# Kernel tuning notes

Measured on AMD Instinct MI355X. Metric: run time of the kernel, lower is better.

Reference implementation:

```python
import jax, jax.numpy as jnp
import numpy as np

CORR_RANGE = 4
N_SEGMENT = 8
SIGMA = 0.1
BETA = 10.0


def setup_inputs() -> dict:
    key = jax.random.key(0)
    x = jax.random.normal(key, (64, 256, 56, 56), dtype=jnp.float32)
    return {"x": x}


def reference(x):
    d = CORR_RANGE
    K = 2 * d + 1  # 9
    bt, c, h, w = x.shape

    # x.detach() + F.normalize(p=2, dim=1)
    xd = jax.lax.stop_gradient(x)
    norm = jnp.sqrt(jnp.sum(xd * xd, axis=1, keepdims=True))
    x_m = xd / jnp.maximum(norm, 1e-12)

    # temporal shift: segment t gets features of segment t-1, segment 0 -> zeros
    x5 = x_m.reshape(-1, N_SEGMENT, c, h, w)
    x_post = jnp.concatenate([jnp.zeros_like(x5[:, :1]), x5[:, :-1]], axis=1)
    x_post = x_post.reshape(bt, c, h, w)

    # correlation: 81-channel cost volume, channel k = dy*K + dx (torch meshgrid 'ij')
    pad = jnp.pad(x_post, ((0, 0), (0, 0), (d, d), (d, d)))
    vols = [jnp.sum(x_m * pad[:, :, dy:dy + h, dx:dx + w], axis=1)
            for dy in range(K) for dx in range(K)]
    r = jnp.stack(vols, axis=1)  # [bt, K*K, h, w]

    conf = jnp.max(r, axis=1, keepdims=True)  # [bt, 1, h, w]

    # gaussian kernel centered at argmax
    xv = r.transpose(0, 2, 3, 1).reshape(bt, h * w, K, K)
    idx = jnp.argmax(xv.reshape(bt, h * w, K * K), axis=-1)  # [bt, hw]
    h_idx = (idx // K - d).astype(jnp.float32)[..., None, None]
    v_idx = (idx % K - d).astype(jnp.float32)[..., None, None]
    grid = jnp.arange(-d, d + 1, dtype=jnp.float32)  # [K]
    x_cord = grid[:, None]  # rows (matches h_grid over dim 2)
    y_cord = grid[None, :]  # cols (matches v_grid over dim 3)
    gauss = jnp.exp(-((x_cord - h_idx) ** 2 + (y_cord - v_idx) ** 2) / (2.0 * SIGMA ** 2))
    xg = gauss * xv  # [bt, hw, K, K]

    flat = xg.reshape(bt, h * w, K * K) * BETA
    s = jnp.sum(flat, axis=-1, keepdims=True) + 1e-12
    p = (flat / s).reshape(bt, h * w, K, K)
    sum_h = jnp.sum(p, axis=3)  # [bt, hw, K]
    sum_w = jnp.sum(p, axis=2)  # [bt, hw, K]
    h_cord = jnp.sum(sum_h * grid, axis=-1)  # [bt, hw]
    v_cord = jnp.sum(sum_w * grid, axis=-1)
    mot = jnp.stack([h_cord, v_cord], axis=-1)  # [bt, hw, 2]
    mot = mot.transpose(0, 2, 1).reshape(bt, 2, h, w)

    return jnp.concatenate([mot, conf], axis=1)  # [bt, 3, h, w]
```

## Files before the change

### kernel.cpp

```cpp
#include <hip/hip_runtime.h>
#include <cfloat>
#include <math.h>

#define BT 64
#define CHN 256
#define HH 56
#define WW 56
#define HW 3136
#define NPIX (BT * HW)

__global__ __launch_bounds__(256) void norm_kernel(const float* __restrict__ x,
                                                   double* __restrict__ invn) {
    __shared__ double part[4][256];
    const int t   = threadIdx.x;
    const int q   = t >> 6;
    const int grp = t & 63;
    const int g0  = blockIdx.x * 256;
    const int gpx = g0 + 4 * grp;
    const int b   = gpx / HW;
    const int yx  = gpx - b * HW;
    const float* xb = x + (size_t)b * (CHN * HW) + (size_t)(q * 64) * HW + yx;
    double s0 = 0.0, s1 = 0.0, s2 = 0.0, s3 = 0.0;
    #pragma unroll 8
    for (int c = 0; c < 64; ++c) {
        float4 v = *(const float4*)(xb + (size_t)c * HW);
        s0 += (double)v.x * (double)v.x;
        s1 += (double)v.y * (double)v.y;
        s2 += (double)v.z * (double)v.z;
        s3 += (double)v.w * (double)v.w;
    }
    part[q][4 * grp + 0] = s0;
    part[q][4 * grp + 1] = s1;
    part[q][4 * grp + 2] = s2;
    part[q][4 * grp + 3] = s3;
    __syncthreads();
    double tt = part[0][t] + part[1][t] + part[2][t] + part[3][t];
    invn[g0 + t] = 1.0 / fmax(sqrt(tt), 1e-12);
}

__device__ __forceinline__ void dma16(const float* g, float* l) {
    __builtin_amdgcn_global_load_lds(
        (const __attribute__((address_space(1))) void*)g,
        (__attribute__((address_space(3))) void*)l, 16, 0, 0);
}

__global__ __launch_bounds__(576, 6) void corr_kernel(const float* __restrict__ x,
                                                      const double* __restrict__ invn,
                                                      float* __restrict__ out) {
    const int tile = blockIdx.x;
    const int b    = blockIdx.y;
    const int offs0 = (tile & 3);
    const int offs1 = (tile >> 2);
    const int x0 = (offs0 < 3) ? offs0 * 16 : 40;
    const int y0 = (offs1 < 3) ? offs1 * 16 : 40;
    const int tid = threadIdx.x;

    float* outb = out + (size_t)b * 3 * HW;

    if ((b & 7) == 0) {
        if (tid < 256) {
            int py = tid >> 4, px = tid & 15;
            int g = (y0 + py) * WW + (x0 + px);
            outb[g] = 0.f; outb[HW + g] = 0.f; outb[2 * HW + g] = 0.f;
        }
        return;
    }

    const int wave = tid >> 6;
    const int lane = tid & 63;
    const int ty  = lane >> 2;
    const int tx4 = lane & 3;

    __shared__ float  xs[2 * 1024];
    __shared__ float  ps[2 * 2304];
    __shared__ double ivq[24 * 25];
    __shared__ double ivp[256];
    __shared__ unsigned long long red[256];

    const float*  xcur    = x    + (size_t)b * (CHN * HW);
    const float*  xprv    = x    + (size_t)(b - 1) * (CHN * HW);
    const double* inv_cur = invn + (size_t)b * HW;
    const double* inv_prv = invn + (size_t)(b - 1) * HW;

    {
        int row = tid / 24, col = tid - row * 24;
        int gy = y0 - 4 + row, gx = x0 - 4 + col;
        double v = 0.0;
        if (gy >= 0 && gy < HH && gx >= 0 && gx < WW) v = inv_prv[gy * WW + gx];
        ivq[row * 25 + col] = v;
    }
    if (tid < 256) {
        ivp[tid] = inv_cur[(y0 + (tid >> 4)) * WW + x0 + (tid & 15)];
        red[tid] = 0ULL;
    }

    int ch_s  = tid / 144;
    int rem_s = tid - ch_s * 144;
    int row_s = rem_s / 6;
    int c4    = rem_s - row_s * 6;
    int gy_s  = y0 - 4 + row_s;
    int gx_s  = x0 - 4 + 4 * c4;
    const bool pv = (gy_s >= 0 && gy_s < HH && gx_s >= 0 && gx_s < WW);
    const size_t ps_g = (size_t)ch_s * HW + (pv ? (gy_s * WW + gx_s) : 0);
    size_t xs_g = 0;
    if (tid < 256) {
        int chx = tid >> 6, r2 = tid & 63, sy = r2 >> 2, sx = r2 & 3;
        xs_g = (size_t)chx * HW + (size_t)(y0 + sy) * WW + x0 + 4 * sx;
    }
    const int wv = tid >> 6;
    float* const ps_w0 = &ps[wv * 256];
    float* const xs_w0 = &xs[wv * 256];

    if (!pv) {
        *(float4*)&ps[tid * 4]        = make_float4(0.f, 0.f, 0.f, 0.f);
        *(float4*)&ps[2304 + tid * 4] = make_float4(0.f, 0.f, 0.f, 0.f);
    }

    if (pv) dma16(xprv + ps_g, ps_w0);
    if (tid < 256) dma16(xcur + xs_g, xs_w0);

    float acc[9][4];
    #pragma unroll
    for (int j = 0; j < 9; ++j)
        #pragma unroll
        for (int t = 0; t < 4; ++t) acc[j][t] = 0.f;

    __syncthreads();

    for (int cc = 0; cc < 64; ++cc) {
        const int cur = cc & 1;
        if (cc < 63) {
            const size_t cb = (size_t)((cc + 1) * 4) * HW;
            const int nxt = cur ^ 1;
            if (pv) dma16(xprv + cb + ps_g, ps_w0 + nxt * 2304);
            if (tid < 256) dma16(xcur + cb + xs_g, xs_w0 + nxt * 1024);
        }

        const float* xb = &xs[cur * 1024 + ty * 16 + 4 * tx4];
        const float* pb = &ps[cur * 2304 + (ty + wave) * 24 + 4 * tx4];
        #pragma unroll
        for (int ch = 0; ch < 4; ++ch) {
            float4 xq = *(const float4*)(xb + ch * 256);
            float4 w0 = *(const float4*)(pb + ch * 576);
            float4 w1 = *(const float4*)(pb + ch * 576 + 4);
            float4 w2 = *(const float4*)(pb + ch * 576 + 8);
            float win[12] = { w0.x, w0.y, w0.z, w0.w,
                              w1.x, w1.y, w1.z, w1.w,
                              w2.x, w2.y, w2.z, w2.w };
            #pragma unroll
            for (int dx = 0; dx < 9; ++dx) {
                acc[dx][0] = fmaf(xq.x, win[dx + 0], acc[dx][0]);
                acc[dx][1] = fmaf(xq.y, win[dx + 1], acc[dx][1]);
                acc[dx][2] = fmaf(xq.z, win[dx + 2], acc[dx][2]);
                acc[dx][3] = fmaf(xq.w, win[dx + 3], acc[dx][3]);
            }
        }
        __syncthreads();
    }

    const int px0 = ty * 16 + 4 * tx4;
    double ip[4];
    #pragma unroll
    for (int t = 0; t < 4; ++t) ip[t] = ivp[px0 + t];
    unsigned long long best[4] = { 0ULL, 0ULL, 0ULL, 0ULL };
    #pragma unroll
    for (int dx = 0; dx < 9; ++dx) {
        #pragma unroll
        for (int t = 0; t < 4; ++t) {
            double qv = ivq[(ty + wave) * 25 + 4 * tx4 + t + dx];
            float rv = (float)((double)acc[dx][t] * ip[t] * qv);
            unsigned int bits = __float_as_uint(rv);
            unsigned int key = (bits & 0x80000000u) ? ~bits : (bits | 0x80000000u);
            unsigned long long pk =
                ((unsigned long long)key << 32) | (unsigned int)(80 - (wave * 9 + dx));
            if (pk > best[t]) best[t] = pk;
        }
    }
    #pragma unroll
    for (int t = 0; t < 4; ++t)
        atomicMax(&red[ty + ((4 * tx4 + t) << 4)], best[t]);
    __syncthreads();

    if (tid < 256) {
        unsigned long long pk = red[(tid >> 4) + ((tid & 15) << 4)];
        int o = 80 - (int)(pk & 0xffffffffu);
        unsigned int key  = (unsigned int)(pk >> 32);
        unsigned int bits = (key & 0x80000000u) ? (key ^ 0x80000000u) : ~key;
        float v = __uint_as_float(bits);
        float h_idx = (float)(o / 9) - 4.f;
        float v_idx = (float)(o - (o / 9) * 9) - 4.f;
        float R  = 10.f * v;
        float pc = R / (R + 1e-12f);
        int py = tid >> 4, pxl = tid & 15;
        int g = (y0 + py) * WW + (x0 + pxl);
        outb[g]          = h_idx * pc;
        outb[HW + g]     = v_idx * pc;
        outb[2 * HW + g] = v;
    }
}

extern "C" void kernel_launch(void* const* d_in, const int* in_sizes, int n_in,
                              void* d_out, int out_size, void* d_ws, size_t ws_size,
                              hipStream_t stream) {
    const float* x = (const float*)d_in[0];
    float* out = (float*)d_out;
    double* invn = (double*)d_ws;

    hipLaunchKernelGGL(norm_kernel, dim3(NPIX / 256), dim3(256), 0, stream,
                       x, invn);
    hipLaunchKernelGGL(corr_kernel, dim3(16, 64), dim3(576), 0, stream,
                       x, invn, out);
}
```

Baseline: 573.7 us.

## Swizzle shared-memory halo layout and split norm reduction across more blocks

The correlation kernel now stores each 6-float4 halo row in shared memory with a per-row rotation, and every thread reads its three window float4s through matching swizzled offsets. This is meant to spread LDS accesses across banks and cut conflicts in the inner loop. Separately, the norm kernel now handles 64 pixels per block with 16 channel slices, giving four times as many blocks and shorter per-thread loops, at the cost of a wider shared-memory reduction.

```diff
diff --git a/kernel.cpp b/kernel.cpp
--- a/kernel.cpp
+++ b/kernel.cpp
@@ -11,31 +11,34 @@
 
 __global__ __launch_bounds__(256) void norm_kernel(const float* __restrict__ x,
                                                    double* __restrict__ invn) {
-    __shared__ double part[4][256];
-    const int t   = threadIdx.x;
-    const int q   = t >> 6;
-    const int grp = t & 63;
-    const int g0  = blockIdx.x * 256;
-    const int gpx = g0 + 4 * grp;
-    const int b   = gpx / HW;
-    const int yx  = gpx - b * HW;
-    const float* xb = x + (size_t)b * (CHN * HW) + (size_t)(q * 64) * HW + yx;
+    __shared__ double part[16][64];
+    const int t  = threadIdx.x;
+    const int sl = t >> 4;
+    const int gp = t & 15;
+    const int g0 = blockIdx.x * 64;
+    const int b  = g0 / HW;
+    const int yx = g0 - b * HW + 4 * gp;
+    const float* xb = x + (size_t)b * (CHN * HW) + (size_t)(sl * 16) * HW + yx;
     double s0 = 0.0, s1 = 0.0, s2 = 0.0, s3 = 0.0;
     #pragma unroll 8
-    for (int c = 0; c < 64; ++c) {
+    for (int c = 0; c < 16; ++c) {
         float4 v = *(const float4*)(xb + (size_t)c * HW);
         s0 += (double)v.x * (double)v.x;
         s1 += (double)v.y * (double)v.y;
         s2 += (double)v.z * (double)v.z;
         s3 += (double)v.w * (double)v.w;
     }
-    part[q][4 * grp + 0] = s0;
-    part[q][4 * grp + 1] = s1;
-    part[q][4 * grp + 2] = s2;
-    part[q][4 * grp + 3] = s3;
+    part[sl][4 * gp + 0] = s0;
+    part[sl][4 * gp + 1] = s1;
+    part[sl][4 * gp + 2] = s2;
+    part[sl][4 * gp + 3] = s3;
     __syncthreads();
-    double tt = part[0][t] + part[1][t] + part[2][t] + part[3][t];
-    invn[g0 + t] = 1.0 / fmax(sqrt(tt), 1e-12);
+    if (t < 64) {
+        double tt = 0.0;
+        #pragma unroll
+        for (int s = 0; s < 16; ++s) tt += part[s][t];
+        invn[g0 + t] = 1.0 / fmax(sqrt(tt), 1e-12);
+    }
 }
 
 __device__ __forceinline__ void dma16(const float* g, float* l) {
@@ -94,12 +97,13 @@
         red[tid] = 0ULL;
     }
 
-    int ch_s  = tid / 144;
-    int rem_s = tid - ch_s * 144;
-    int row_s = rem_s / 6;
-    int c4    = rem_s - row_s * 6;
-    int gy_s  = y0 - 4 + row_s;
-    int gx_s  = x0 - 4 + 4 * c4;
+    int ch_s   = tid / 144;
+    int rem_s  = tid - ch_s * 144;
+    int r_slot = rem_s / 6;
+    int c_slot = rem_s - r_slot * 6;
+    int c4     = c_slot - (r_slot % 6); if (c4 < 0) c4 += 6;
+    int gy_s   = y0 - 4 + r_slot;
+    int gx_s   = x0 - 4 + 4 * c4;
     const bool pv = (gy_s >= 0 && gy_s < HH && gx_s >= 0 && gx_s < WW);
     const size_t ps_g = (size_t)ch_s * HW + (pv ? (gy_s * WW + gx_s) : 0);
     size_t xs_g = 0;
@@ -114,6 +118,17 @@
     if (!pv) {
         *(float4*)&ps[tid * 4]        = make_float4(0.f, 0.f, 0.f, 0.f);
         *(float4*)&ps[2304 + tid * 4] = make_float4(0.f, 0.f, 0.f, 0.f);
+    }
+
+    const int R = ty + wave;
+    int sb0, sb1, sb2;
+    {
+        int m0 = (tx4 + 0 + R) % 6;
+        int m1 = (tx4 + 1 + R) % 6;
+        int m2 = (tx4 + 2 + R) % 6;
+        sb0 = (6 * R + m0) * 4;
+        sb1 = (6 * R + m1) * 4;
+        sb2 = (6 * R + m2) * 4;
     }
 
     if (pv) dma16(xprv + ps_g, ps_w0);
@@ -137,13 +152,13 @@
         }
 
         const float* xb = &xs[cur * 1024 + ty * 16 + 4 * tx4];
-        const float* pb = &ps[cur * 2304 + (ty + wave) * 24 + 4 * tx4];
+        const float* pc = &ps[cur * 2304];
         #pragma unroll
         for (int ch = 0; ch < 4; ++ch) {
             float4 xq = *(const float4*)(xb + ch * 256);
-            float4 w0 = *(const float4*)(pb + ch * 576);
-            float4 w1 = *(const float4*)(pb + ch * 576 + 4);
-            float4 w2 = *(const float4*)(pb + ch * 576 + 8);
+            float4 w0 = *(const float4*)(pc + ch * 576 + sb0);
+            float4 w1 = *(const float4*)(pc + ch * 576 + sb1);
+            float4 w2 = *(const float4*)(pc + ch * 576 + sb2);
             float win[12] = { w0.x, w0.y, w0.z, w0.w,
                               w1.x, w1.y, w1.z, w1.w,
                               w2.x, w2.y, w2.z, w2.w };
@@ -167,7 +182,7 @@
     for (int dx = 0; dx < 9; ++dx) {
         #pragma unroll
         for (int t = 0; t < 4; ++t) {
-            double qv = ivq[(ty + wave) * 25 + 4 * tx4 + t + dx];
+            double qv = ivq[R * 25 + 4 * tx4 + t + dx];
             float rv = (float)((double)acc[dx][t] * ip[t] * qv);
             unsigned int bits = __float_as_uint(rv);
             unsigned int key = (bits & 0x80000000u) ? ~bits : (bits | 0x80000000u);
@@ -189,12 +204,12 @@
         float v = __uint_as_float(bits);
         float h_idx = (float)(o / 9) - 4.f;
         float v_idx = (float)(o - (o / 9) * 9) - 4.f;
-        float R  = 10.f * v;
-        float pc = R / (R + 1e-12f);
+        float R2  = 10.f * v;
+        float pc2 = R2 / (R2 + 1e-12f);
         int py = tid >> 4, pxl = tid & 15;
         int g = (y0 + py) * WW + (x0 + pxl);
-        outb[g]          = h_idx * pc;
-        outb[HW + g]     = v_idx * pc;
+        outb[g]          = h_idx * pc2;
+        outb[HW + g]     = v_idx * pc2;
         outb[2 * HW + g] = v;
     }
 }
@@ -206,7 +221,7 @@
     float* out = (float*)d_out;
     double* invn = (double*)d_ws;
 
-    hipLaunchKernelGGL(norm_kernel, dim3(NPIX / 256), dim3(256), 0, stream,
+    hipLaunchKernelGGL(norm_kernel, dim3(NPIX / 64), dim3(256), 0, stream,
                        x, invn);
     hipLaunchKernelGGL(corr_kernel, dim3(16, 64), dim3(576), 0, stream,
                        x, invn, out);
```

Result: slower. 713.5 us (+24.4%).

## Fuse L2-norm computation into correlation kernel using LDS-staged tiles

Applied to the files above, without the earlier changes.

Drops the separate norm kernel and its workspace buffer. Each correlation block now accumulates per-pixel sums of squares in double precision from the tiles it already stages in LDS, for both the current and the previous frame. After the channel loop it reduces these sums and builds the inverse-norm tables in shared memory. This avoids a second full pass over the input and an extra kernel launch, at the cost of extra fp64 FMAs and LDS reads in the main loop, plus norms recomputed for halo pixels shared by neighbouring tiles.

```diff
diff --git a/kernel.cpp b/kernel.cpp
--- a/kernel.cpp
+++ b/kernel.cpp
@@ -9,35 +9,6 @@
 #define HW 3136
 #define NPIX (BT * HW)
 
-__global__ __launch_bounds__(256) void norm_kernel(const float* __restrict__ x,
-                                                   double* __restrict__ invn) {
-    __shared__ double part[4][256];
-    const int t   = threadIdx.x;
-    const int q   = t >> 6;
-    const int grp = t & 63;
-    const int g0  = blockIdx.x * 256;
-    const int gpx = g0 + 4 * grp;
-    const int b   = gpx / HW;
-    const int yx  = gpx - b * HW;
-    const float* xb = x + (size_t)b * (CHN * HW) + (size_t)(q * 64) * HW + yx;
-    double s0 = 0.0, s1 = 0.0, s2 = 0.0, s3 = 0.0;
-    #pragma unroll 8
-    for (int c = 0; c < 64; ++c) {
-        float4 v = *(const float4*)(xb + (size_t)c * HW);
-        s0 += (double)v.x * (double)v.x;
-        s1 += (double)v.y * (double)v.y;
-        s2 += (double)v.z * (double)v.z;
-        s3 += (double)v.w * (double)v.w;
-    }
-    part[q][4 * grp + 0] = s0;
-    part[q][4 * grp + 1] = s1;
-    part[q][4 * grp + 2] = s2;
-    part[q][4 * grp + 3] = s3;
-    __syncthreads();
-    double tt = part[0][t] + part[1][t] + part[2][t] + part[3][t];
-    invn[g0 + t] = 1.0 / fmax(sqrt(tt), 1e-12);
-}
-
 __device__ __forceinline__ void dma16(const float* g, float* l) {
     __builtin_amdgcn_global_load_lds(
         (const __attribute__((address_space(1))) void*)g,
@@ -45,7 +16,6 @@
 }
 
 __global__ __launch_bounds__(576, 6) void corr_kernel(const float* __restrict__ x,
-                                                      const double* __restrict__ invn,
                                                       float* __restrict__ out) {
     const int tile = blockIdx.x;
     const int b    = blockIdx.y;
@@ -77,22 +47,10 @@
     __shared__ double ivp[256];
     __shared__ unsigned long long red[256];
 
-    const float*  xcur    = x    + (size_t)b * (CHN * HW);
-    const float*  xprv    = x    + (size_t)(b - 1) * (CHN * HW);
-    const double* inv_cur = invn + (size_t)b * HW;
-    const double* inv_prv = invn + (size_t)(b - 1) * HW;
-
-    {
-        int row = tid / 24, col = tid - row * 24;
-        int gy = y0 - 4 + row, gx = x0 - 4 + col;
-        double v = 0.0;
-        if (gy >= 0 && gy < HH && gx >= 0 && gx < WW) v = inv_prv[gy * WW + gx];
-        ivq[row * 25 + col] = v;
-    }
-    if (tid < 256) {
-        ivp[tid] = inv_cur[(y0 + (tid >> 4)) * WW + x0 + (tid & 15)];
-        red[tid] = 0ULL;
-    }
+    const float*  xcur = x + (size_t)b * (CHN * HW);
+    const float*  xprv = x + (size_t)(b - 1) * (CHN * HW);
+
+    if (tid < 256) red[tid] = 0ULL;
 
     int ch_s  = tid / 144;
     int rem_s = tid - ch_s * 144;
@@ -125,6 +83,9 @@
         #pragma unroll
         for (int t = 0; t < 4; ++t) acc[j][t] = 0.f;
 
+    double sqp0 = 0.0, sqp1 = 0.0, sqp2 = 0.0, sqp3 = 0.0;
+    double sqx0 = 0.0, sqx1 = 0.0, sqx2 = 0.0, sqx3 = 0.0;
+
     __syncthreads();
 
     for (int cc = 0; cc < 64; ++cc) {
@@ -134,6 +95,21 @@
             const int nxt = cur ^ 1;
             if (pv) dma16(xprv + cb + ps_g, ps_w0 + nxt * 2304);
             if (tid < 256) dma16(xcur + cb + xs_g, xs_w0 + nxt * 1024);
+        }
+
+        {
+            float4 rb = *(const float4*)&ps[cur * 2304 + tid * 4];
+            sqp0 = fma((double)rb.x, (double)rb.x, sqp0);
+            sqp1 = fma((double)rb.y, (double)rb.y, sqp1);
+            sqp2 = fma((double)rb.z, (double)rb.z, sqp2);
+            sqp3 = fma((double)rb.w, (double)rb.w, sqp3);
+        }
+        if (tid < 256) {
+            float4 rb = *(const float4*)&xs[cur * 1024 + tid * 4];
+            sqx0 = fma((double)rb.x, (double)rb.x, sqx0);
+            sqx1 = fma((double)rb.y, (double)rb.y, sqx1);
+            sqx2 = fma((double)rb.z, (double)rb.z, sqx2);
+            sqx3 = fma((double)rb.w, (double)rb.w, sqx3);
         }
 
         const float* xb = &xs[cur * 1024 + ty * 16 + 4 * tx4];
@@ -158,6 +134,35 @@
         __syncthreads();
     }
 
+    double* psq = (double*)ps;
+    double* xsq = (double*)xs;
+    psq[tid * 4 + 0] = sqp0;
+    psq[tid * 4 + 1] = sqp1;
+    psq[tid * 4 + 2] = sqp2;
+    psq[tid * 4 + 3] = sqp3;
+    if (tid < 256) {
+        xsq[tid * 4 + 0] = sqx0;
+        xsq[tid * 4 + 1] = sqx1;
+        xsq[tid * 4 + 2] = sqx2;
+        xsq[tid * 4 + 3] = sqx3;
+    }
+    __syncthreads();
+    {
+        int hr = tid / 24, hc = tid - hr * 24;
+        int gy = y0 - 4 + hr, gx = x0 - 4 + hc;
+        int sl = (hr * 6 + (hc >> 2)) * 4 + (hc & 3);
+        double s = psq[sl] + psq[576 + sl] + psq[1152 + sl] + psq[1728 + sl];
+        ivq[hr * 25 + hc] = (gy >= 0 && gy < HH && gx >= 0 && gx < WW)
+                          ? 1.0 / fmax(sqrt(s), 1e-12) : 0.0;
+    }
+    if (tid < 256) {
+        int r = tid >> 4, c = tid & 15;
+        int sl = (r * 4 + (c >> 2)) * 4 + (c & 3);
+        double s = xsq[sl] + xsq[256 + sl] + xsq[512 + sl] + xsq[768 + sl];
+        ivp[tid] = 1.0 / fmax(sqrt(s), 1e-12);
+    }
+    __syncthreads();
+
     const int px0 = ty * 16 + 4 * tx4;
     double ip[4];
     #pragma unroll
@@ -189,12 +194,12 @@
         float v = __uint_as_float(bits);
         float h_idx = (float)(o / 9) - 4.f;
         float v_idx = (float)(o - (o / 9) * 9) - 4.f;
-        float R  = 10.f * v;
-        float pc = R / (R + 1e-12f);
+        float R2  = 10.f * v;
+        float pc2 = R2 / (R2 + 1e-12f);
         int py = tid >> 4, pxl = tid & 15;
         int g = (y0 + py) * WW + (x0 + pxl);
-        outb[g]          = h_idx * pc;
-        outb[HW + g]     = v_idx * pc;
+        outb[g]          = h_idx * pc2;
+        outb[HW + g]     = v_idx * pc2;
         outb[2 * HW + g] = v;
     }
 }
@@ -204,10 +209,8 @@
                               hipStream_t stream) {
     const float* x = (const float*)d_in[0];
     float* out = (float*)d_out;
-    double* invn = (double*)d_ws;
-
-    hipLaunchKernelGGL(norm_kernel, dim3(NPIX / 256), dim3(256), 0, stream,
-                       x, invn);
+    (void)d_ws; (void)ws_size;
+
     hipLaunchKernelGGL(corr_kernel, dim3(16, 64), dim3(576), 0, stream,
-                       x, invn, out);
+                       x, out);
 }
```

Measured after the change: 949.8 us. 65.6% more time.

## Split norm reduction across channel blocks with atomic double accumulation

Applied to the files above, without the earlier changes.

Replaces the per-pixel norm kernel with a sum-of-squares kernel that splits the channel dimension into 8 blocks of 32 and accumulates partial sums into a zeroed workspace with double atomicAdd. The inverse sqrt is moved into the correlation kernel's shared-memory setup. This is meant to raise parallelism and per-thread streaming in the norm pass, but it adds a memset launch and double-precision atomics on global memory, and summation order is no longer deterministic.

```diff
diff --git a/kernel.cpp b/kernel.cpp
--- a/kernel.cpp
+++ b/kernel.cpp
@@ -9,33 +9,26 @@
 #define HW 3136
 #define NPIX (BT * HW)
 
-__global__ __launch_bounds__(256) void norm_kernel(const float* __restrict__ x,
-                                                   double* __restrict__ invn) {
-    __shared__ double part[4][256];
-    const int t   = threadIdx.x;
-    const int q   = t >> 6;
-    const int grp = t & 63;
-    const int g0  = blockIdx.x * 256;
-    const int gpx = g0 + 4 * grp;
-    const int b   = gpx / HW;
-    const int yx  = gpx - b * HW;
-    const float* xb = x + (size_t)b * (CHN * HW) + (size_t)(q * 64) * HW + yx;
+__global__ __launch_bounds__(784) void sumsq_kernel(const float* __restrict__ x,
+                                                    double* __restrict__ sq) {
+    const int g = threadIdx.x;
+    const int q = blockIdx.x;
+    const int b = blockIdx.y;
+    const float* xb = x + (size_t)b * (CHN * HW) + (size_t)(q * 32) * HW + 4 * g;
     double s0 = 0.0, s1 = 0.0, s2 = 0.0, s3 = 0.0;
     #pragma unroll 8
-    for (int c = 0; c < 64; ++c) {
+    for (int c = 0; c < 32; ++c) {
         float4 v = *(const float4*)(xb + (size_t)c * HW);
-        s0 += (double)v.x * (double)v.x;
-        s1 += (double)v.y * (double)v.y;
-        s2 += (double)v.z * (double)v.z;
-        s3 += (double)v.w * (double)v.w;
-    }
-    part[q][4 * grp + 0] = s0;
-    part[q][4 * grp + 1] = s1;
-    part[q][4 * grp + 2] = s2;
-    part[q][4 * grp + 3] = s3;
-    __syncthreads();
-    double tt = part[0][t] + part[1][t] + part[2][t] + part[3][t];
-    invn[g0 + t] = 1.0 / fmax(sqrt(tt), 1e-12);
+        s0 = fma((double)v.x, (double)v.x, s0);
+        s1 = fma((double)v.y, (double)v.y, s1);
+        s2 = fma((double)v.z, (double)v.z, s2);
+        s3 = fma((double)v.w, (double)v.w, s3);
+    }
+    double* d = sq + (size_t)b * HW + 4 * g;
+    atomicAdd(d + 0, s0);
+    atomicAdd(d + 1, s1);
+    atomicAdd(d + 2, s2);
+    atomicAdd(d + 3, s3);
 }
 
 __device__ __forceinline__ void dma16(const float* g, float* l) {
@@ -45,7 +38,7 @@
 }
 
 __global__ __launch_bounds__(576, 6) void corr_kernel(const float* __restrict__ x,
-                                                      const double* __restrict__ invn,
+                                                      const double* __restrict__ sq,
                                                       float* __restrict__ out) {
     const int tile = blockIdx.x;
     const int b    = blockIdx.y;
@@ -77,20 +70,21 @@
     __shared__ double ivp[256];
     __shared__ unsigned long long red[256];
 
-    const float*  xcur    = x    + (size_t)b * (CHN * HW);
-    const float*  xprv    = x    + (size_t)(b - 1) * (CHN * HW);
-    const double* inv_cur = invn + (size_t)b * HW;
-    const double* inv_prv = invn + (size_t)(b - 1) * HW;
+    const float*  xcur   = x  + (size_t)b * (CHN * HW);
+    const float*  xprv   = x  + (size_t)(b - 1) * (CHN * HW);
+    const double* sq_cur = sq + (size_t)b * HW;
+    const double* sq_prv = sq + (size_t)(b - 1) * HW;
 
     {
         int row = tid / 24, col = tid - row * 24;
         int gy = y0 - 4 + row, gx = x0 - 4 + col;
         double v = 0.0;
-        if (gy >= 0 && gy < HH && gx >= 0 && gx < WW) v = inv_prv[gy * WW + gx];
+        if (gy >= 0 && gy < HH && gx >= 0 && gx < WW)
+            v = 1.0 / fmax(sqrt(sq_prv[gy * WW + gx]), 1e-12);
         ivq[row * 25 + col] = v;
     }
     if (tid < 256) {
-        ivp[tid] = inv_cur[(y0 + (tid >> 4)) * WW + x0 + (tid & 15)];
+        ivp[tid] = 1.0 / fmax(sqrt(sq_cur[(y0 + (tid >> 4)) * WW + x0 + (tid & 15)]), 1e-12);
         red[tid] = 0ULL;
     }
 
@@ -189,12 +183,12 @@
         float v = __uint_as_float(bits);
         float h_idx = (float)(o / 9) - 4.f;
         float v_idx = (float)(o - (o / 9) * 9) - 4.f;
-        float R  = 10.f * v;
-        float pc = R / (R + 1e-12f);
+        float R2  = 10.f * v;
+        float pc2 = R2 / (R2 + 1e-12f);
         int py = tid >> 4, pxl = tid & 15;
         int g = (y0 + py) * WW + (x0 + pxl);
-        outb[g]          = h_idx * pc;
-        outb[HW + g]     = v_idx * pc;
+        outb[g]          = h_idx * pc2;
+        outb[HW + g]     = v_idx * pc2;
         outb[2 * HW + g] = v;
     }
 }
@@ -204,10 +198,11 @@
                               hipStream_t stream) {
     const float* x = (const float*)d_in[0];
     float* out = (float*)d_out;
-    double* invn = (double*)d_ws;
-
-    hipLaunchKernelGGL(norm_kernel, dim3(NPIX / 256), dim3(256), 0, stream,
-                       x, invn);
+    double* sq = (double*)d_ws;
+
+    hipMemsetAsync(d_ws, 0, (size_t)NPIX * sizeof(double), stream);
+    hipLaunchKernelGGL(sumsq_kernel, dim3(8, 64), dim3(784), 0, stream,
+                       x, sq);
     hipLaunchKernelGGL(corr_kernel, dim3(16, 64), dim3(576), 0, stream,
-                       x, invn, out);
-}
+                       x, sq, out);
+}
```

Result: slower. 585.8 us (+2.1%).
